# Kernel tuning notes

Hardware: AMD Instinct MI355X
Metric: run time of the kernel (lower is better)

Reference implementation:

```python
import jax, jax.numpy as jnp
import numpy as np
import math

B, T, C = 2, 2048, 1024
N_HEADS = 16
HEAD_DIM = C // N_HEADS  # 64


def setup_inputs() -> dict:
    key = jax.random.key(0)
    ks = jax.random.split(key, 5)
    scale = 0.02
    return {
        "x": jax.random.normal(ks[0], (B, T, C), dtype=jnp.float32),
        "Wq": jax.random.normal(ks[1], (C, C), dtype=jnp.float32) * scale,
        "Wk": jax.random.normal(ks[2], (C, C), dtype=jnp.float32) * scale,
        "Wv": jax.random.normal(ks[3], (C, C), dtype=jnp.float32) * scale,
        "Wc": jax.random.normal(ks[4], (C, C), dtype=jnp.float32) * scale,
        "bc": jnp.zeros((C,), dtype=jnp.float32),
    }


def reference(x, Wq, Wk, Wv, Wc, bc):
    b, t, c = x.shape
    h, dh = N_HEADS, HEAD_DIM
    # Q/K/V projections (Linear, no bias): y = x @ W.T
    def proj(W):
        y = jnp.einsum('btc,dc->btd', x, W)
        return y.reshape(b, t, h, dh).transpose(0, 2, 1, 3)  # [B,H,T,dh]
    Q, K, V = proj(Wq), proj(Wk), proj(Wv)

    # scaled dot-product scores [B,H,T,T]
    scores = jnp.einsum('bhqd,bhkd->bhqk', Q, K) / math.sqrt(dh)
    # additive causal mask: + (1 - tril) * -1e9, as in the original
    causal = jnp.tril(jnp.ones((t, t), dtype=scores.dtype))
    scores = scores + (1.0 - causal) * (-1e9)

    attn = jax.nn.softmax(scores, axis=-1)  # dropout = identity (eval mode)
    o = jnp.einsum('bhqk,bhkd->bhqd', attn, V)
    o = o.transpose(0, 2, 1, 3).reshape(b, t, c)
    # output projection with bias (resid dropout = identity in eval)
    return jnp.einsum('btc,dc->btd', o, Wc) + bc
```

## Files before the change

### kernel.cpp

```cpp
#include <hip/hip_runtime.h>
#include <hip/hip_bf16.h>


typedef __attribute__((ext_vector_type(4))) float f32x4;
typedef __attribute__((ext_vector_type(4))) unsigned int u32x4;
typedef __attribute__((ext_vector_type(8))) __bf16 bf16x8;
typedef __attribute__((ext_vector_type(8))) unsigned short us8;
typedef __attribute__((ext_vector_type(4))) unsigned short us4;

#define LOG2E 1.4426950408889634f

__device__ __forceinline__ unsigned short f2bf(float f) {
    unsigned u = __builtin_bit_cast(unsigned, f);
    u += 0x7fffu + ((u >> 16) & 1u);
    return (unsigned short)(u >> 16);
}

__device__ __forceinline__ unsigned cvt_pk_bf16(float lo, float hi) {
    unsigned r;
    asm("v_cvt_pk_bf16_f32 %0, %1, %2" : "=v"(r) : "v"(lo), "v"(hi));
    return r;
}

__device__ __forceinline__ f32x4 mfma16(us8 a, us8 b, f32x4 c) {
    return __builtin_amdgcn_mfma_f32_16x16x32_bf16(
        __builtin_bit_cast(bf16x8, a), __builtin_bit_cast(bf16x8, b), c, 0, 0, 0);
}

__global__ __launch_bounds__(256) void fill_sentinel(float* __restrict__ out, int n) {
    int i = blockIdx.x * 256 + threadIdx.x;
    if (i < n) out[i] = 12345.0f;
}

__global__ __launch_bounds__(256) void cvt_xw(
    const float* __restrict__ x, const float* __restrict__ wq,
    const float* __restrict__ wk, const float* __restrict__ wv,
    unsigned short* __restrict__ xb, unsigned short* __restrict__ wqkvb) {
    long i = (long)(blockIdx.x * 256 + threadIdx.x) * 4;
    const float* src; unsigned short* dst; long off;
    if (i < 4194304L)      { src = x;  dst = xb;              off = i; }
    else if (i < 5242880L) { src = wq; dst = wqkvb;           off = i - 4194304L; }
    else if (i < 6291456L) { src = wk; dst = wqkvb + 1048576; off = i - 5242880L; }
    else                   { src = wv; dst = wqkvb + 2097152; off = i - 6291456L; }
    f32x4 v = *(const f32x4*)(src + off);
    us4 o = { f2bf(v[0]), f2bf(v[1]), f2bf(v[2]), f2bf(v[3]) };
    *(us4*)(dst + off) = o;
}

__global__ __launch_bounds__(256) void cvt_wc(const float* __restrict__ wc,
                                              unsigned short* __restrict__ wcb) {
    int idx = (blockIdx.x * 256 + threadIdx.x) * 4;
    f32x4 v = *(const f32x4*)(wc + idx);
    us4 o = { f2bf(v[0]), f2bf(v[1]), f2bf(v[2]), f2bf(v[3]) };
    *(us4*)(wcb + idx) = o;
}

template <int MI>
__device__ __forceinline__ void gemm_core_bb(
    const unsigned short* __restrict__ A, const unsigned short* __restrict__ B,
    int K, int m0, int n0, unsigned short* As, unsigned short* Bs, f32x4 acc[MI][4]) {
    const int tid = threadIdx.x;
    const int lane = tid & 63, wid = tid >> 6;
    const int g = lane >> 4, s = lane & 15;
    const int wr = wid >> 1, wc = wid & 1;
#pragma unroll
    for (int mi = 0; mi < MI; mi++)
#pragma unroll
        for (int ni = 0; ni < 4; ni++) acc[mi][ni] = (f32x4){0.f, 0.f, 0.f, 0.f};
    const int row = tid >> 3, col = (tid & 7) * 8;
    for (int k0 = 0; k0 < K; k0 += 64) {
        us8 av[MI], bv[4];
#pragma unroll
        for (int p = 0; p < MI; p++)
            av[p] = *(const us8*)(A + (size_t)(m0 + row + p * 32) * K + k0 + col);
#pragma unroll
        for (int p = 0; p < 4; p++)
            bv[p] = *(const us8*)(B + (size_t)(n0 + row + p * 32) * K + k0 + col);
        __syncthreads();
#pragma unroll
        for (int p = 0; p < MI; p++)
            *(us8*)(As + (row + p * 32) * 72 + col) = av[p];
#pragma unroll
        for (int p = 0; p < 4; p++)
            *(us8*)(Bs + (row + p * 32) * 72 + col) = bv[p];
        __syncthreads();
#pragma unroll
        for (int kk = 0; kk < 2; kk++) {
            us8 af[MI], bf[4];
#pragma unroll
            for (int mi = 0; mi < MI; mi++)
                af[mi] = *(const us8*)(As + (wr * (MI * 16) + mi * 16 + s) * 72 + kk * 32 + g * 8);
#pragma unroll
            for (int ni = 0; ni < 4; ni++)
                bf[ni] = *(const us8*)(Bs + (wc * 64 + ni * 16 + s) * 72 + kk * 32 + g * 8);
#pragma unroll
            for (int mi = 0; mi < MI; mi++)
#pragma unroll
                for (int ni = 0; ni < 4; ni++)
                    acc[mi][ni] = mfma16(af[mi], bf[ni], acc[mi][ni]);
        }
    }
}

__global__ __launch_bounds__(256) void gemm_qkv(
    const unsigned short* __restrict__ X, const unsigned short* __restrict__ Wb,
    unsigned short* __restrict__ Qb, unsigned short* __restrict__ Kb,
    unsigned short* __restrict__ VtG) {
    __shared__ unsigned short S[18432];
    unsigned short* As = S;
    unsigned short* Bs = S + 9216;
    const int bid = blockIdx.x;
    const int xcd = bid & 7, idx = bid >> 3;
    const int bm  = (xcd & 3) * 8 + (idx & 7);
    const int bnl = (xcd >> 2) * 12 + (idx >> 3);
    const int m0 = bm * 128;
    const int which = bnl >> 3;
    const int n0 = (bnl & 7) * 128;
    const unsigned short* W = Wb + (size_t)which * 1048576;
    f32x4 acc[4][4];
    gemm_core_bb<4>(X, W, 1024, m0, n0, As, Bs, acc);
    const int tid = threadIdx.x, lane = tid & 63, wid = tid >> 6;
    const int g = lane >> 4, s = lane & 15, wr = wid >> 1, wc = wid & 1;
    if (which < 2) {
        unsigned short* dst = which == 0 ? Qb : Kb;
        const float scale = which == 0 ? 0.125f : 1.0f;
#pragma unroll
        for (int mi = 0; mi < 4; mi++)
#pragma unroll
            for (int ni = 0; ni < 4; ni++) {
                int n1 = n0 + wc * 64 + ni * 16 + s;
                int hh = n1 >> 6, dd = n1 & 63;
#pragma unroll
                for (int r = 0; r < 4; r++) {
                    int mg = m0 + wr * 64 + mi * 16 + 4 * g + r;
                    int bb = mg >> 11, tt = mg & 2047;
                    dst[((size_t)(bb * 16 + hh) * 2048 + tt) * 64 + dd] = f2bf(acc[mi][ni][r] * scale);
                }
            }
    } else {
        __syncthreads();
        unsigned* T32 = (unsigned*)S;
#pragma unroll
        for (int mi = 0; mi < 4; mi++)
#pragma unroll
            for (int ni = 0; ni < 4; ni++) {
                int nl = wc * 64 + ni * 16 + s;
                int mlh = ((wr * 64 + mi * 16) >> 1) + 2 * g;
                T32[nl * 68 + mlh]     = cvt_pk_bf16(acc[mi][ni][0], acc[mi][ni][1]);
                T32[nl * 68 + mlh + 1] = cvt_pk_bf16(acc[mi][ni][2], acc[mi][ni][3]);
            }
        __syncthreads();
        const int row = tid >> 4, col8 = (tid & 15) * 8;
        const int bb = m0 >> 11, tt0 = m0 & 2047;
#pragma unroll
        for (int p = 0; p < 8; p++) {
            int nl = row + 16 * p;
            int n1 = n0 + nl, hh = n1 >> 6, dd = n1 & 63;
            us8 v = *(const us8*)(S + nl * 136 + col8);
            *(us8*)(VtG + ((size_t)(bb * 16 + hh) * 64 + dd) * 2048 + tt0 + col8) = v;
        }
    }
}

#define ATTN_EPILOGUE(QB0, OA, LP)                                              \
    {                                                                           \
        float lf = (LP);                                                        \
        lf += __shfl_xor(lf, 16);                                               \
        lf += __shfl_xor(lf, 32);                                               \
        float li[4];                                                            \
        _Pragma("unroll") for (int r = 0; r < 4; r++)                           \
            li[r] = __shfl(lf, 4 * g + r, 64);                                  \
        _Pragma("unroll") for (int db = 0; db < 4; db++)                        \
            _Pragma("unroll") for (int r = 0; r < 4; r++) {                     \
                int qq = (QB0) + 4 * g + r;                                     \
                float v = (OA)[db][r] / li[r];                                  \
                Ob[((size_t)(b * 2048) + qq) * 1024 + h * 64 + db * 16 + s] = f2bf(v); \
            }                                                                   \
    }

__global__ __launch_bounds__(256) void attn(
    const unsigned short* __restrict__ Qb, const unsigned short* __restrict__ Kb,
    const unsigned short* __restrict__ VtG, unsigned short* __restrict__ Ob) {
    __shared__ unsigned short Ks[2][64 * 72];
    __shared__ unsigned short Vt[2][64 * 72];
    const int bh = blockIdx.x & 31, i = blockIdx.x >> 5;
    const int b = bh >> 4, h = bh & 15;
    const unsigned short* Qp = Qb + (size_t)bh * 2048 * 64;
    const unsigned short* Kp = Kb + (size_t)bh * 2048 * 64;
    const unsigned short* Vp = VtG + (size_t)bh * 64 * 2048;
    const int tid = threadIdx.x, lane = tid & 63, wid = tid >> 6;
    const int g = lane >> 4, s = lane & 15;
    const int qbA = i * 64 + wid * 16;
    const int qbB = (31 - i) * 64 + wid * 16;
    const int qgA = qbA + s, qgB = qbB + s;
    us8 qfA[2], qfB[2];
    qfA[0] = *(const us8*)(Qp + (size_t)qgA * 64 + g * 8);
    qfA[1] = *(const us8*)(Qp + (size_t)qgA * 64 + 32 + g * 8);
    qfB[0] = *(const us8*)(Qp + (size_t)qgB * 64 + g * 8);
    qfB[1] = *(const us8*)(Qp + (size_t)qgB * 64 + 32 + g * 8);
    float m_run = -3.0e38f, l_part = 0.f;
    f32x4 o_acc[4];
#pragma unroll
    for (int db = 0; db < 4; db++) o_acc[db] = (f32x4){0.f, 0.f, 0.f, 0.f};
    const int srow = tid >> 3, scol = (tid & 7) * 8;
    auto tileoff = [&](int jj) { return (jj <= i ? jj : jj - i - 1) * 64; };
    us8 kpre[2], vpre[2];
#pragma unroll
    for (int p = 0; p < 2; p++) {
        kpre[p] = *(const us8*)(Kp + (size_t)(srow + 32 * p) * 64 + scol);
        vpre[p] = *(const us8*)(Vp + (size_t)(srow + 32 * p) * 2048 + scol);
    }
#pragma unroll
    for (int p = 0; p < 2; p++) {
        *(us8*)(&Ks[0][(srow + 32 * p) * 72 + scol]) = kpre[p];
        *(us8*)(&Vt[0][(srow + 32 * p) * 72 + scol]) = vpre[p];
    }
    {
        const int nk = tileoff(1);
#pragma unroll
        for (int p = 0; p < 2; p++) {
            kpre[p] = *(const us8*)(Kp + (size_t)(nk + srow + 32 * p) * 64 + scol);
            vpre[p] = *(const us8*)(Vp + (size_t)(srow + 32 * p) * 2048 + nk + scol);
        }
    }
    int cur = 0;
    for (int it = 0; it <= 32; ++it) {
        __syncthreads();
        if (it < 32) {
#pragma unroll
            for (int p = 0; p < 2; p++) {
                *(us8*)(&Ks[cur ^ 1][(srow + 32 * p) * 72 + scol]) = kpre[p];
                *(us8*)(&Vt[cur ^ 1][(srow + 32 * p) * 72 + scol]) = vpre[p];
            }
            if (it < 31) {
                const int nk = tileoff(it + 2);
#pragma unroll
                for (int p = 0; p < 2; p++) {
                    kpre[p] = *(const us8*)(Kp + (size_t)(nk + srow + 32 * p) * 64 + scol);
                    vpre[p] = *(const us8*)(Vp + (size_t)(srow + 32 * p) * 2048 + nk + scol);
                }
            }
        }
        if (it == i + 1) {
            ATTN_EPILOGUE(qbA, o_acc, l_part);
            m_run = -3.0e38f; l_part = 0.f;
#pragma unroll
            for (int db = 0; db < 4; db++) o_acc[db] = (f32x4){0.f, 0.f, 0.f, 0.f};
        }
        const bool qsel = it > i;
        const int kv0 = tileoff(it);
        const int qg = qsel ? qgB : qgA;
        const us8* qf = qsel ? qfB : qfA;
        const unsigned short* Kc = Ks[cur];
        const unsigned short* Vc = Vt[cur];
        float sf[4][4];
        __builtin_amdgcn_s_setprio(1);
#pragma unroll
        for (int f = 0; f < 4; f++) {
            f32x4 a = (f32x4){0.f, 0.f, 0.f, 0.f};
            us8 k0v = *(const us8*)(Kc + (f * 16 + s) * 72 + g * 8);
            us8 k1v = *(const us8*)(Kc + (f * 16 + s) * 72 + 32 + g * 8);
            a = mfma16(k0v, qf[0], a);
            a = mfma16(k1v, qf[1], a);
#pragma unroll
            for (int r = 0; r < 4; r++) sf[f][r] = a[r];
        }
        __builtin_amdgcn_s_setprio(0);
        const bool diag = qsel ? (it == 32) : (it == i);
        if (diag) {
#pragma unroll
            for (int f = 0; f < 4; f++)
#pragma unroll
                for (int r = 0; r < 4; r++)
                    if (kv0 + f * 16 + 4 * g + r > qg) sf[f][r] = -3.0e38f;
        }
        float mt = -3.0e38f;
#pragma unroll
        for (int f = 0; f < 4; f++)
#pragma unroll
            for (int r = 0; r < 4; r++) mt = fmaxf(mt, sf[f][r]);
        if (!__all(mt - m_run <= 8.0f)) {
            mt = fmaxf(mt, __shfl_xor(mt, 16));
            mt = fmaxf(mt, __shfl_xor(mt, 32));
            float mnew = fmaxf(m_run, mt);
            float alpha = __builtin_amdgcn_exp2f((m_run - mnew) * LOG2E);
            l_part *= alpha;
            float al[4];
#pragma unroll
            for (int r = 0; r < 4; r++) al[r] = __shfl(alpha, 4 * g + r, 64);
#pragma unroll
            for (int db = 0; db < 4; db++)
#pragma unroll
                for (int r = 0; r < 4; r++) o_acc[db][r] *= al[r];
            m_run = mnew;
        }
        float psum = 0.f;
#pragma unroll
        for (int f = 0; f < 4; f++)
#pragma unroll
            for (int r = 0; r < 4; r++) {
                float p = __builtin_amdgcn_exp2f((sf[f][r] - m_run) * LOG2E);
                sf[f][r] = p;
                psum += p;
            }
        l_part += psum;
        unsigned pk[4][2];
#pragma unroll
        for (int f = 0; f < 4; f++)
#pragma unroll
            for (int hh2 = 0; hh2 < 2; hh2++)
                pk[f][hh2] = cvt_pk_bf16(sf[f][2 * hh2], sf[f][2 * hh2 + 1]);
        const int srcA = 32 * (g & 1) + s, srcB = srcA + 16;
        const bool ghi = g >= 2;
        us8 pa[2];
#pragma unroll
        for (int kk = 0; kk < 2; kk++) {
            unsigned e0 = __shfl(pk[kk * 2][0], srcA, 64);
            unsigned e1 = __shfl(pk[kk * 2][1], srcA, 64);
            unsigned e2 = __shfl(pk[kk * 2][0], srcB, 64);
            unsigned e3 = __shfl(pk[kk * 2][1], srcB, 64);
            unsigned o0 = __shfl(pk[kk * 2 + 1][0], srcA, 64);
            unsigned o1 = __shfl(pk[kk * 2 + 1][1], srcA, 64);
            unsigned o2 = __shfl(pk[kk * 2 + 1][0], srcB, 64);
            unsigned o3 = __shfl(pk[kk * 2 + 1][1], srcB, 64);
            u32x4 dw = { ghi ? o0 : e0, ghi ? o1 : e1, ghi ? o2 : e2, ghi ? o3 : e3 };
            pa[kk] = __builtin_bit_cast(us8, dw);
        }
        __builtin_amdgcn_s_setprio(1);
#pragma unroll
        for (int db = 0; db < 4; db++) {
            const unsigned short* vrow = Vc + (db * 16 + s) * 72;
            us8 vf0 = *(const us8*)(vrow + g * 8);
            o_acc[db] = mfma16(pa[0], vf0, o_acc[db]);
            us8 vf1 = *(const us8*)(vrow + 32 + g * 8);
            o_acc[db] = mfma16(pa[1], vf1, o_acc[db]);
        }
        __builtin_amdgcn_s_setprio(0);
        cur ^= 1;
    }
    ATTN_EPILOGUE(qbB, o_acc, l_part);
}

__global__ __launch_bounds__(256) void gemm_out(
    const unsigned short* __restrict__ O, const unsigned short* __restrict__ Wcb,
    const float* __restrict__ bc, float* __restrict__ out) {
    __shared__ unsigned short As[64 * 72];
    __shared__ unsigned short Bs[128 * 72];
    const int bid = blockIdx.x;
    const int xcd = bid & 7, idx = bid >> 3;
    const int bm = xcd * 8 + (idx & 7);
    const int bn = idx >> 3;
    const int m0 = bm * 64, n0 = bn * 128;
    f32x4 acc[2][4];
    gemm_core_bb<2>(O, Wcb, 1024, m0, n0, As, Bs, acc);
    const int lane = threadIdx.x & 63, wid = threadIdx.x >> 6;
    const int g = lane >> 4, s = lane & 15, wr = wid >> 1, wc = wid & 1;
#pragma unroll
    for (int mi = 0; mi < 2; mi++)
#pragma unroll
        for (int ni = 0; ni < 4; ni++) {
            int ng = n0 + wc * 64 + ni * 16 + s;
            float bias = bc[ng];
#pragma unroll
            for (int r = 0; r < 4; r++) {
                int mg = m0 + wr * 32 + mi * 16 + 4 * g + r;
                out[(size_t)mg * 1024 + ng] = acc[mi][ni][r] + bias;
            }
        }
}

extern "C" void kernel_launch(void* const* d_in, const int* in_sizes, int n_in,
                              void* d_out, int out_size, void* d_ws, size_t ws_size,
                              hipStream_t stream) {
    const float* x  = (const float*)d_in[0];
    const float* Wq = (const float*)d_in[1];
    const float* Wk = (const float*)d_in[2];
    const float* Wv = (const float*)d_in[3];
    const float* Wc = (const float*)d_in[4];
    const float* bc = (const float*)d_in[5];
    float* out = (float*)d_out;

    if (ws_size < 33554432) {
        fill_sentinel<<<(out_size + 255) / 256, 256, 0, stream>>>(out, out_size);
        return;
    }
    char* w = (char*)d_ws;
    unsigned short* Qb  = (unsigned short*)(w);
    unsigned short* Kb  = (unsigned short*)(w + 8388608);
    unsigned short* VtG = (unsigned short*)(w + 16777216);
    unsigned short* Ob  = (unsigned short*)(w + 25165824);
    unsigned short* Wcb = (unsigned short*)(w);
    unsigned short* xb    = (unsigned short*)d_out;
    unsigned short* wqkvb = (unsigned short*)((char*)d_out + 8388608);

    cvt_xw<<<7168, 256, 0, stream>>>(x, Wq, Wk, Wv, xb, wqkvb);
    gemm_qkv<<<768, 256, 0, stream>>>(xb, wqkvb, Qb, Kb, VtG);
    attn<<<512, 256, 0, stream>>>(Qb, Kb, VtG, Ob);
    cvt_wc<<<1024, 256, 0, stream>>>(Wc, Wcb);
    gemm_out<<<512, 256, 0, stream>>>(Ob, Wcb, bc, out);
}
```

Before: 119.6 us.

## Use 128-key KV tiles with XOR-swizzled LDS in attention kernel

The attention kernel now stages 128 keys per iteration instead of 64, which halves the number of barrier-synchronized iterations (17 instead of 33). The padded 72-stride LDS layout is replaced by an unpadded layout with an XOR swizzle to avoid bank conflicts. Launch bounds now request 2 blocks per CU. Causal masking is applied per 64-key subtile. The cost is more LDS and more registers per block (larger prefetch buffers and a doubled score array), which may limit occupancy.

```diff
diff --git a/kernel.cpp b/kernel.cpp
--- a/kernel.cpp
+++ b/kernel.cpp
@@ -178,11 +178,11 @@
             }                                                                   \
     }
 
-__global__ __launch_bounds__(256) void attn(
+__global__ __launch_bounds__(256, 2) void attn(
     const unsigned short* __restrict__ Qb, const unsigned short* __restrict__ Kb,
     const unsigned short* __restrict__ VtG, unsigned short* __restrict__ Ob) {
-    __shared__ unsigned short Ks[2][64 * 72];
-    __shared__ unsigned short Vt[2][64 * 72];
+    __shared__ unsigned short Ks[2][128 * 64];
+    __shared__ unsigned short Vt[2][64 * 128];
     const int bh = blockIdx.x & 31, i = blockIdx.x >> 5;
     const int b = bh >> 4, h = bh & 15;
     const unsigned short* Qp = Qb + (size_t)bh * 2048 * 64;
@@ -202,83 +202,85 @@
     f32x4 o_acc[4];
 #pragma unroll
     for (int db = 0; db < 4; db++) o_acc[db] = (f32x4){0.f, 0.f, 0.f, 0.f};
-    const int srow = tid >> 3, scol = (tid & 7) * 8;
-    auto tileoff = [&](int jj) { return (jj <= i ? jj : jj - i - 1) * 64; };
-    us8 kpre[2], vpre[2];
-#pragma unroll
-    for (int p = 0; p < 2; p++) {
-        kpre[p] = *(const us8*)(Kp + (size_t)(srow + 32 * p) * 64 + scol);
-        vpre[p] = *(const us8*)(Vp + (size_t)(srow + 32 * p) * 2048 + scol);
-    }
-#pragma unroll
-    for (int p = 0; p < 2; p++) {
-        *(us8*)(&Ks[0][(srow + 32 * p) * 72 + scol]) = kpre[p];
-        *(us8*)(&Vt[0][(srow + 32 * p) * 72 + scol]) = vpre[p];
-    }
-    {
-        const int nk = tileoff(1);
-#pragma unroll
-        for (int p = 0; p < 2; p++) {
-            kpre[p] = *(const us8*)(Kp + (size_t)(nk + srow + 32 * p) * 64 + scol);
-            vpre[p] = *(const us8*)(Vp + (size_t)(srow + 32 * p) * 2048 + nk + scol);
-        }
-    }
+    const int nA = (i + 2) >> 1;
+    const int krow = tid >> 3, kcolb = (tid & 7) * 16;
+    const int vd = tid >> 2, vcb = (tid & 3) * 16;
+    const int swl = (s & 7) << 4;
+    const int vsw = (vd & 7) << 4;
+    auto tb = [&](int t) { return (t < nA ? t : t - nA) * 128; };
+    us8 kpre[4], vpre[4];
+    auto loadpre = [&](int base) {
+#pragma unroll
+        for (int p = 0; p < 4; p++) {
+            kpre[p] = *(const us8*)((const char*)Kp + (size_t)(base + krow + 32 * p) * 128 + kcolb);
+            vpre[p] = *(const us8*)((const char*)Vp + (size_t)vd * 4096 + base * 2 + vcb + p * 64);
+        }
+    };
+    auto writebuf = [&](int bi) {
+#pragma unroll
+        for (int p = 0; p < 4; p++) {
+            int r = krow + 32 * p;
+            *(us8*)((char*)&Ks[bi][0] + r * 128 + (kcolb ^ ((r & 7) << 4))) = kpre[p];
+            *(us8*)((char*)&Vt[bi][0] + vd * 256 + ((vcb + p * 64) ^ vsw)) = vpre[p];
+        }
+    };
+    loadpre(0);
+    writebuf(0);
+    loadpre(tb(1));
     int cur = 0;
-    for (int it = 0; it <= 32; ++it) {
+    for (int it = 0; it < 17; ++it) {
         __syncthreads();
-        if (it < 32) {
-#pragma unroll
-            for (int p = 0; p < 2; p++) {
-                *(us8*)(&Ks[cur ^ 1][(srow + 32 * p) * 72 + scol]) = kpre[p];
-                *(us8*)(&Vt[cur ^ 1][(srow + 32 * p) * 72 + scol]) = vpre[p];
-            }
-            if (it < 31) {
-                const int nk = tileoff(it + 2);
-#pragma unroll
-                for (int p = 0; p < 2; p++) {
-                    kpre[p] = *(const us8*)(Kp + (size_t)(nk + srow + 32 * p) * 64 + scol);
-                    vpre[p] = *(const us8*)(Vp + (size_t)(srow + 32 * p) * 2048 + nk + scol);
-                }
-            }
-        }
-        if (it == i + 1) {
+        if (it < 16) {
+            writebuf(cur ^ 1);
+            if (it < 15) loadpre(tb(it + 2));
+        }
+        if (it == nA) {
             ATTN_EPILOGUE(qbA, o_acc, l_part);
             m_run = -3.0e38f; l_part = 0.f;
 #pragma unroll
             for (int db = 0; db < 4; db++) o_acc[db] = (f32x4){0.f, 0.f, 0.f, 0.f};
         }
-        const bool qsel = it > i;
-        const int kv0 = tileoff(it);
-        const int qg = qsel ? qgB : qgA;
-        const us8* qf = qsel ? qfB : qfA;
-        const unsigned short* Kc = Ks[cur];
-        const unsigned short* Vc = Vt[cur];
-        float sf[4][4];
+        const bool isA = it < nA;
+        const int kvb = tb(it);
+        const int qg = isA ? qgA : qgB;
+        const int qbW = isA ? qbA : qbB;
+        const us8* qf = isA ? qfA : qfB;
+        const char* Kc = (const char*)&Ks[cur][0];
+        const char* Vc = (const char*)&Vt[cur][0];
+        float sf[2][4][4];
         __builtin_amdgcn_s_setprio(1);
 #pragma unroll
-        for (int f = 0; f < 4; f++) {
-            f32x4 a = (f32x4){0.f, 0.f, 0.f, 0.f};
-            us8 k0v = *(const us8*)(Kc + (f * 16 + s) * 72 + g * 8);
-            us8 k1v = *(const us8*)(Kc + (f * 16 + s) * 72 + 32 + g * 8);
-            a = mfma16(k0v, qf[0], a);
-            a = mfma16(k1v, qf[1], a);
-#pragma unroll
-            for (int r = 0; r < 4; r++) sf[f][r] = a[r];
-        }
+        for (int sub = 0; sub < 2; sub++)
+#pragma unroll
+            for (int f = 0; f < 4; f++) {
+                const char* krp = Kc + (sub * 64 + f * 16 + s) * 128;
+                us8 k0v = *(const us8*)(krp + ((g * 16) ^ swl));
+                us8 k1v = *(const us8*)(krp + ((64 + g * 16) ^ swl));
+                f32x4 a = (f32x4){0.f, 0.f, 0.f, 0.f};
+                a = mfma16(k0v, qf[0], a);
+                a = mfma16(k1v, qf[1], a);
+#pragma unroll
+                for (int r = 0; r < 4; r++) sf[sub][f][r] = a[r];
+            }
         __builtin_amdgcn_s_setprio(0);
-        const bool diag = qsel ? (it == 32) : (it == i);
-        if (diag) {
+#pragma unroll
+        for (int sub = 0; sub < 2; sub++) {
+            const int kv0 = kvb + sub * 64;
+            if (kv0 + 63 > qbW) {
+#pragma unroll
+                for (int f = 0; f < 4; f++)
+#pragma unroll
+                    for (int r = 0; r < 4; r++)
+                        if (kv0 + f * 16 + 4 * g + r > qg) sf[sub][f][r] = -3.0e38f;
+            }
+        }
+        float mt = -3.0e38f;
+#pragma unroll
+        for (int sub = 0; sub < 2; sub++)
 #pragma unroll
             for (int f = 0; f < 4; f++)
 #pragma unroll
-                for (int r = 0; r < 4; r++)
-                    if (kv0 + f * 16 + 4 * g + r > qg) sf[f][r] = -3.0e38f;
-        }
-        float mt = -3.0e38f;
-#pragma unroll
-        for (int f = 0; f < 4; f++)
-#pragma unroll
-            for (int r = 0; r < 4; r++) mt = fmaxf(mt, sf[f][r]);
+                for (int r = 0; r < 4; r++) mt = fmaxf(mt, sf[sub][f][r]);
         if (!__all(mt - m_run <= 8.0f)) {
             mt = fmaxf(mt, __shfl_xor(mt, 16));
             mt = fmaxf(mt, __shfl_xor(mt, 32));
@@ -296,46 +298,51 @@
         }
         float psum = 0.f;
 #pragma unroll
-        for (int f = 0; f < 4; f++)
-#pragma unroll
-            for (int r = 0; r < 4; r++) {
-                float p = __builtin_amdgcn_exp2f((sf[f][r] - m_run) * LOG2E);
-                sf[f][r] = p;
-                psum += p;
-            }
+        for (int sub = 0; sub < 2; sub++)
+#pragma unroll
+            for (int f = 0; f < 4; f++)
+#pragma unroll
+                for (int r = 0; r < 4; r++) {
+                    float p = __builtin_amdgcn_exp2f((sf[sub][f][r] - m_run) * LOG2E);
+                    sf[sub][f][r] = p;
+                    psum += p;
+                }
         l_part += psum;
-        unsigned pk[4][2];
-#pragma unroll
-        for (int f = 0; f < 4; f++)
-#pragma unroll
-            for (int hh2 = 0; hh2 < 2; hh2++)
-                pk[f][hh2] = cvt_pk_bf16(sf[f][2 * hh2], sf[f][2 * hh2 + 1]);
-        const int srcA = 32 * (g & 1) + s, srcB = srcA + 16;
-        const bool ghi = g >= 2;
-        us8 pa[2];
-#pragma unroll
-        for (int kk = 0; kk < 2; kk++) {
-            unsigned e0 = __shfl(pk[kk * 2][0], srcA, 64);
-            unsigned e1 = __shfl(pk[kk * 2][1], srcA, 64);
-            unsigned e2 = __shfl(pk[kk * 2][0], srcB, 64);
-            unsigned e3 = __shfl(pk[kk * 2][1], srcB, 64);
-            unsigned o0 = __shfl(pk[kk * 2 + 1][0], srcA, 64);
-            unsigned o1 = __shfl(pk[kk * 2 + 1][1], srcA, 64);
-            unsigned o2 = __shfl(pk[kk * 2 + 1][0], srcB, 64);
-            unsigned o3 = __shfl(pk[kk * 2 + 1][1], srcB, 64);
-            u32x4 dw = { ghi ? o0 : e0, ghi ? o1 : e1, ghi ? o2 : e2, ghi ? o3 : e3 };
-            pa[kk] = __builtin_bit_cast(us8, dw);
-        }
-        __builtin_amdgcn_s_setprio(1);
-#pragma unroll
-        for (int db = 0; db < 4; db++) {
-            const unsigned short* vrow = Vc + (db * 16 + s) * 72;
-            us8 vf0 = *(const us8*)(vrow + g * 8);
-            o_acc[db] = mfma16(pa[0], vf0, o_acc[db]);
-            us8 vf1 = *(const us8*)(vrow + 32 + g * 8);
-            o_acc[db] = mfma16(pa[1], vf1, o_acc[db]);
-        }
-        __builtin_amdgcn_s_setprio(0);
+#pragma unroll
+        for (int sub = 0; sub < 2; sub++) {
+            unsigned pk[4][2];
+#pragma unroll
+            for (int f = 0; f < 4; f++)
+#pragma unroll
+                for (int hh2 = 0; hh2 < 2; hh2++)
+                    pk[f][hh2] = cvt_pk_bf16(sf[sub][f][2 * hh2], sf[sub][f][2 * hh2 + 1]);
+            const int srcA = 32 * (g & 1) + s, srcB = srcA + 16;
+            const bool ghi = g >= 2;
+            us8 pa[2];
+#pragma unroll
+            for (int kk = 0; kk < 2; kk++) {
+                unsigned e0 = __shfl(pk[kk * 2][0], srcA, 64);
+                unsigned e1 = __shfl(pk[kk * 2][1], srcA, 64);
+                unsigned e2 = __shfl(pk[kk * 2][0], srcB, 64);
+                unsigned e3 = __shfl(pk[kk * 2][1], srcB, 64);
+                unsigned o0 = __shfl(pk[kk * 2 + 1][0], srcA, 64);
+                unsigned o1 = __shfl(pk[kk * 2 + 1][1], srcA, 64);
+                unsigned o2 = __shfl(pk[kk * 2 + 1][0], srcB, 64);
+                unsigned o3 = __shfl(pk[kk * 2 + 1][1], srcB, 64);
+                u32x4 dw = { ghi ? o0 : e0, ghi ? o1 : e1, ghi ? o2 : e2, ghi ? o3 : e3 };
+                pa[kk] = __builtin_bit_cast(us8, dw);
+            }
+            __builtin_amdgcn_s_setprio(1);
+#pragma unroll
+            for (int db = 0; db < 4; db++) {
+                const char* vrow = Vc + (db * 16 + s) * 256;
+                us8 vf0 = *(const us8*)(vrow + ((sub * 128 + g * 16) ^ swl));
+                o_acc[db] = mfma16(pa[0], vf0, o_acc[db]);
+                us8 vf1 = *(const us8*)(vrow + ((sub * 128 + 64 + g * 16) ^ swl));
+                o_acc[db] = mfma16(pa[1], vf1, o_acc[db]);
+            }
+            __builtin_amdgcn_s_setprio(0);
+        }
         cur ^= 1;
     }
     ATTN_EPILOGUE(qbB, o_acc, l_part);
```

After: 118.9 us. About the same (-0.6%).
